# Kernel tuning notes

Measured on AMD Instinct MI355X. Metric: run time of the kernel, lower is better.

The kernel has to match this reference:

```python
import jax, jax.numpy as jnp
import numpy as np

B, S, HID = 4, 2048, 2048
H, KV, D = 16, 4, 128
G = H // KV  # kv groups
EPS = 1e-6
SCALE = D ** -0.5


def setup_inputs() -> dict:
    key = jax.random.key(0)
    ks = jax.random.split(key, 8)
    hidden_states = jax.random.normal(ks[0], (B, S, HID), jnp.float32)
    # real RoPE tables (rotate-half convention: freqs duplicated across halves)
    inv_freq = 1.0 / (10000.0 ** (np.arange(0, D, 2, dtype=np.float32) / D))
    t = np.arange(S, dtype=np.float32)
    freqs = np.outer(t, inv_freq)                      # [S, D/2]
    emb = np.concatenate([freqs, freqs], axis=-1)      # [S, D]
    cos = jnp.asarray(np.cos(emb), jnp.float32)
    sin = jnp.asarray(np.sin(emb), jnp.float32)
    std = HID ** -0.5
    Wq = jax.random.normal(ks[1], (HID, H * D), jnp.float32) * std
    Wk = jax.random.normal(ks[2], (HID, KV * D), jnp.float32) * std
    Wv = jax.random.normal(ks[3], (HID, KV * D), jnp.float32) * std
    Wo = jax.random.normal(ks[4], (H * D, HID), jnp.float32) * std
    q_norm_w = jnp.ones((D,), jnp.float32)
    k_norm_w = jnp.ones((D,), jnp.float32)
    return {"hidden_states": hidden_states, "cos": cos, "sin": sin,
            "Wq": Wq, "Wk": Wk, "Wv": Wv, "Wo": Wo,
            "q_norm_w": q_norm_w, "k_norm_w": k_norm_w}


def _rms_norm(x, w):
    xf = x.astype(jnp.float32)
    var = jnp.mean(xf * xf, axis=-1, keepdims=True)
    return w * (xf * jax.lax.rsqrt(var + EPS)).astype(x.dtype)


def _rotate_half(x):
    x1, x2 = x[..., : D // 2], x[..., D // 2:]
    return jnp.concatenate([-x2, x1], axis=-1)


def reference(hidden_states, cos, sin, Wq, Wk, Wv, Wo, q_norm_w, k_norm_w):
    x = hidden_states  # [B, S, HID]
    # projections + per-head RMSNorm
    q = _rms_norm((x @ Wq).reshape(B, S, H, D), q_norm_w).transpose(0, 2, 1, 3)   # [B,H,S,D]
    k = _rms_norm((x @ Wk).reshape(B, S, KV, D), k_norm_w).transpose(0, 2, 1, 3)  # [B,KV,S,D]
    v = (x @ Wv).reshape(B, S, KV, D).transpose(0, 2, 1, 3)                        # [B,KV,S,D]
    # RoPE (cos/sin broadcast [S,D] -> [B,heads,S,D])
    q = q * cos + _rotate_half(q) * sin
    k = k * cos + _rotate_half(k) * sin
    # GQA attention without materializing expanded K/V: group q heads per kv head
    qg = q.reshape(B, KV, G, S, D)
    scores = jnp.einsum('bkgsd,bktd->bkgst', qg, k) * SCALE       # [B,KV,G,S,S]
    probs = jax.nn.softmax(scores, axis=-1)
    out = jnp.einsum('bkgst,bktd->bkgsd', probs, v)               # [B,KV,G,S,D]
    out = out.reshape(B, H, S, D).transpose(0, 2, 1, 3).reshape(B, S, H * D)
    return out @ Wo
```

## Files before the change

kernel.cpp:

```cpp
#include <hip/hip_runtime.h>

#define DEVI __device__ __forceinline__

#define B_    4
#define S_    2048
#define HID_  2048
#define H_    16
#define KV_   4
#define D_    128
#define NQKV_ 3072
#define SCALE_ 0.08838834764831845f
#define L2E_   1.44269504088896340736f

typedef __bf16 bf16x8 __attribute__((ext_vector_type(8)));
typedef float  f32x4  __attribute__((ext_vector_type(4)));
typedef float  f32x16 __attribute__((ext_vector_type(16)));
typedef unsigned short ushort_t;

DEVI unsigned short f2bu(float f) {
  unsigned u = __float_as_uint(f);
  u += 0x7fffu + ((u >> 16) & 1u);
  return (unsigned short)(u >> 16);
}
DEVI float bu2f(unsigned short s) { return __uint_as_float(((unsigned)s) << 16); }
DEVI unsigned pk2(float a, float b) {
  return (unsigned)f2bu(a) | ((unsigned)f2bu(b) << 16);
}

DEVI void storev(ushort_t* p, float v) { *p = f2bu(v); }
DEVI void storev(float* p, float v)    { *p = v; }

DEVI void gl_lds16(const void* gptr, void* ldsptr) {
  __builtin_amdgcn_global_load_lds(
      (const __attribute__((address_space(1))) void*)gptr,
      (__attribute__((address_space(3))) void*)ldsptr, 16, 0, 0);
}

__global__ void k_cvt(const float* __restrict__ in, ushort_t* __restrict__ out, int n8) {
  int i = blockIdx.x * blockDim.x + threadIdx.x;
  if (i >= n8) return;
  const float4* p = (const float4*)in + (size_t)i * 2;
  float4 a = p[0], b = p[1];
  uint4 o;
  o.x = pk2(a.x, a.y);
  o.y = pk2(a.z, a.w);
  o.z = pk2(b.x, b.y);
  o.w = pk2(b.z, b.w);
  ((uint4*)out)[i] = o;
}

__global__ void k_transw(const float* __restrict__ in, ushort_t* __restrict__ out,
                         int K, int N) {
  __shared__ float tile[64][65];
  int k0 = blockIdx.x * 64, n0 = blockIdx.y * 64;
  int c = threadIdx.x & 63, r0 = threadIdx.x >> 6;
  #pragma unroll
  for (int i = 0; i < 16; ++i) {
    int r = r0 * 16 + i;
    tile[r][c] = in[(size_t)(k0 + r) * N + n0 + c];
  }
  __syncthreads();
  #pragma unroll
  for (int i = 0; i < 16; ++i) {
    int r = r0 * 16 + i;
    out[(size_t)(n0 + r) * K + k0 + c] = f2bu(tile[c][r]);
  }
}

__global__ void k_vtrans(const ushort_t* __restrict__ qkv, ushort_t* __restrict__ Vt) {
  __shared__ ushort_t tile[64][65];
  int s0 = blockIdx.x * 64, d0 = blockIdx.y * 64;
  int bkv = blockIdx.z, b = bkv >> 2, vh = bkv & 3;
  int c = threadIdx.x & 63, r0 = (threadIdx.x >> 6) * 16;
  const ushort_t* src = qkv + (size_t)(b * S_ + s0) * NQKV_ + 2560 + vh * 128 + d0;
  #pragma unroll
  for (int i = 0; i < 16; ++i) {
    int r = r0 + i;
    tile[r][c] = src[(size_t)r * NQKV_ + c];
  }
  __syncthreads();
  ushort_t* dst = Vt + ((size_t)(b * KV_ + vh) * D_ + d0) * S_ + s0;
  #pragma unroll
  for (int i = 0; i < 16; ++i) {
    int r = r0 + i;
    dst[(size_t)r * S_ + c] = tile[c][r];
  }
}

template <typename OutT>
__global__ __launch_bounds__(256)
void k_gemm(const ushort_t* __restrict__ A, const ushort_t* __restrict__ Bt,
            OutT* __restrict__ C, int M, int N, int K) {
  __shared__ __align__(16) ushort_t As[128 * 64];
  __shared__ __align__(16) ushort_t Bs[128 * 64];
  const int tid = threadIdx.x;
  const int wave = tid >> 6, lane = tid & 63;
  const int wr = wave >> 1, wc = wave & 1;
  const int h4 = lane >> 4, c16 = lane & 15;
  const int m0 = blockIdx.x * 128, n0 = blockIdx.y * 128;

  const int srow  = wave * 8 + (lane >> 3);
  const int scolb = (lane & 7) * 16;

  const ushort_t* Ap = A  + (size_t)m0 * K;
  const ushort_t* Bp = Bt + (size_t)n0 * K;

  f32x4 acc[4][4] = {};

  for (int kt = 0; kt < K; kt += 64) {
    __syncthreads();
    #pragma unroll
    for (int p = 0; p < 4; ++p) {
      int row = p * 32 + srow;
      gl_lds16((const char*)(Ap + (size_t)row * K + kt) + scolb,
               (char*)As + p * 4096 + wave * 1024);
      gl_lds16((const char*)(Bp + (size_t)row * K + kt) + scolb,
               (char*)Bs + p * 4096 + wave * 1024);
    }
    __syncthreads();
    #pragma unroll
    for (int kc = 0; kc < 2; ++kc) {
      bf16x8 af[4], bfr[4];
      #pragma unroll
      for (int m = 0; m < 4; ++m)
        af[m] = *(const bf16x8*)((const char*)As + (wr * 64 + m * 16 + c16) * 128 + kc * 64 + h4 * 16);
      #pragma unroll
      for (int n = 0; n < 4; ++n)
        bfr[n] = *(const bf16x8*)((const char*)Bs + (wc * 64 + n * 16 + c16) * 128 + kc * 64 + h4 * 16);
      #pragma unroll
      for (int m = 0; m < 4; ++m)
        #pragma unroll
        for (int n = 0; n < 4; ++n)
          acc[m][n] = __builtin_amdgcn_mfma_f32_16x16x32_bf16(af[m], bfr[n], acc[m][n], 0, 0, 0);
    }
  }
  #pragma unroll
  for (int m = 0; m < 4; ++m)
    #pragma unroll
    for (int n = 0; n < 4; ++n)
      #pragma unroll
      for (int r = 0; r < 4; ++r) {
        int grow = m0 + wr * 64 + m * 16 + h4 * 4 + r;
        int gcol = n0 + wc * 64 + n * 16 + c16;
        storev(&C[(size_t)grow * N + gcol], acc[m][n][r]);
      }
}

__global__ void k_normrope(const ushort_t* __restrict__ qkv,
                           const float* __restrict__ cosT, const float* __restrict__ sinT,
                           const float* __restrict__ qw, const float* __restrict__ kw,
                           ushort_t* __restrict__ Qr,
                           ushort_t* __restrict__ Kr) {
  int wid = blockIdx.x * 4 + (threadIdx.x >> 6);
  int lane = threadIdx.x & 63;
  int sub = wid % 20;
  int bs = wid / 20;
  int b = bs >> 11, s = bs & 2047;
  bool isQ = sub < 16;
  int head = isQ ? sub : sub - 16;
  const ushort_t* rp = qkv + (size_t)bs * NQKV_ + (isQ ? head * 128 : 2048 + head * 128);
  float e0 = bu2f(rp[lane]);
  float e1 = bu2f(rp[lane + 64]);
  float ss2 = e0 * e0 + e1 * e1;
  #pragma unroll
  for (int off = 32; off; off >>= 1) ss2 += __shfl_xor(ss2, off);
  float rinv = rsqrtf(ss2 * (1.0f / 128.0f) + 1e-6f);
  const float* w = isQ ? qw : kw;
  float y0 = e0 * rinv * w[lane];
  float y1 = e1 * rinv * w[lane + 64];
  float c0 = cosT[s * 128 + lane],      sn0 = sinT[s * 128 + lane];
  float c1 = cosT[s * 128 + lane + 64], sn1 = sinT[s * 128 + lane + 64];
  float o0 = y0 * c0 - y1 * sn0;
  float o1 = y1 * c1 + y0 * sn1;
  if (isQ) { o0 *= (SCALE_ * L2E_); o1 *= (SCALE_ * L2E_); }
  ushort_t* op = isQ ? (Qr + ((size_t)(b * H_ + head) * S_ + s) * D_)
                     : (Kr + ((size_t)(b * KV_ + head) * S_ + s) * D_);
  op[lane]      = f2bu(o0);
  op[lane + 64] = f2bu(o1);
}

__global__ __launch_bounds__(256, 2)
void k_attn(const ushort_t* __restrict__ Qr, const ushort_t* __restrict__ Kr,
            const ushort_t* __restrict__ Vt, ushort_t* __restrict__ AO) {
  __shared__ __align__(16) ushort_t Ks[2][64 * 128];
  __shared__ __align__(16) ushort_t Vs[2][128 * 64];
  const int bh = blockIdx.y;
  const int b = bh >> 4, h = bh & 15, kvh = h >> 2;
  const int q0 = blockIdx.x * 128;
  const int tid = threadIdx.x;
  const int wave = tid >> 6, lane = tid & 63;
  const int l31 = lane & 31, hi = lane >> 5;

  const ushort_t* qp = Qr + ((size_t)(b * H_ + h) * S_ + q0 + wave * 32 + l31) * D_;
  bf16x8 qf[8];
  #pragma unroll
  for (int kc = 0; kc < 8; ++kc)
    qf[kc] = *(const bf16x8*)(qp + kc * 16 + hi * 8);

  const ushort_t* Kg = Kr + (size_t)(b * KV_ + kvh) * S_ * D_;
  const ushort_t* Vg = Vt + (size_t)(b * KV_ + kvh) * D_ * S_;

  const int soff = wave * 1024 + lane * 16;

  float mrow = -1e30f, lsum = 0.0f;
  f32x16 Of[4] = {};

#define STAGE(bufi, s0)                                                        \
  {                                                                            \
    _Pragma("unroll")                                                          \
    for (int p = 0; p < 4; ++p) {                                              \
      int off = p * 4096 + soff;                                               \
      int krow = off >> 8, kcolb = off & 255;                                  \
      int ksc = kcolb ^ ((krow & 7) << 4);                                     \
      gl_lds16((const char*)(Kg + (size_t)((s0) + krow) * D_) + ksc,           \
               (char*)Ks[bufi] + p * 4096 + wave * 1024);                      \
      int vrow = off >> 7, vcolb = off & 127;                                  \
      int vsc = vcolb ^ ((vrow & 7) << 4);                                     \
      gl_lds16((const char*)(Vg + (size_t)vrow * S_ + (s0)) + vsc,             \
               (char*)Vs[bufi] + p * 4096 + wave * 1024);                      \
    }                                                                          \
  }

  STAGE(0, 0);
  asm volatile("s_waitcnt vmcnt(0)" ::: "memory");
  __builtin_amdgcn_s_barrier();

  for (int nt = 0; nt < S_ / 64; ++nt) {
    const int cur = nt & 1;
    if (nt + 1 < S_ / 64) STAGE(cur ^ 1, (nt + 1) * 64);

    f32x16 st[2] = {};
    __builtin_amdgcn_s_setprio(1);
    #pragma unroll
    for (int t = 0; t < 2; ++t) {
      const int row = t * 32 + l31;
      const int xr = (row & 7) << 4;
      #pragma unroll
      for (int kc = 0; kc < 8; ++kc) {
        bf16x8 kf = *(const bf16x8*)((const char*)Ks[cur] + row * 256 +
                                     ((kc * 32 + hi * 16) ^ xr));
        st[t] = __builtin_amdgcn_mfma_f32_32x32x16_bf16(kf, qf[kc], st[t], 0, 0, 0);
      }
    }
    __builtin_amdgcn_s_setprio(0);

    float tmax = st[0][0];
    #pragma unroll
    for (int r = 1; r < 16; ++r) tmax = fmaxf(tmax, st[0][r]);
    #pragma unroll
    for (int r = 0; r < 16; ++r) tmax = fmaxf(tmax, st[1][r]);
    tmax = fmaxf(tmax, __shfl_xor(tmax, 32));

    if (!__all(tmax - mrow <= 8.0f)) {
      const float mnew = fmaxf(mrow, tmax);
      const float corr = exp2f(mrow - mnew);
      #pragma unroll
      for (int dt = 0; dt < 4; ++dt)
        #pragma unroll
        for (int r = 0; r < 16; ++r) Of[dt][r] *= corr;
      lsum *= corr;
      mrow = mnew;
    }

    float psum = 0.0f;
    unsigned u[16];
    #pragma unroll
    for (int t = 0; t < 2; ++t)
      #pragma unroll
      for (int j = 0; j < 8; ++j) {
        float pa = exp2f(st[t][2 * j]     - mrow);
        float pb = exp2f(st[t][2 * j + 1] - mrow);
        psum += pa + pb;
        unsigned short xa = __builtin_bit_cast(unsigned short, (__bf16)pa);
        unsigned short xb = __builtin_bit_cast(unsigned short, (__bf16)pb);
        u[t * 8 + j] = (unsigned)xa | ((unsigned)xb << 16);
      }
    lsum += psum;

    #pragma unroll
    for (int kt = 0; kt < 4; ++kt) {
      const int base = (kt >> 1) * 8 + (kt & 1) * 4;
      unsigned w0 = u[base], w1 = u[base + 1], w2 = u[base + 2], w3 = u[base + 3];
      asm("v_permlane32_swap_b32 %0, %1" : "+v"(w0), "+v"(w2));
      asm("v_permlane32_swap_b32 %0, %1" : "+v"(w1), "+v"(w3));
      uint4 pw; pw.x = w0; pw.y = w1; pw.z = w2; pw.w = w3;
      bf16x8 pb = __builtin_bit_cast(bf16x8, pw);
      __builtin_amdgcn_s_setprio(1);
      #pragma unroll
      for (int dt = 0; dt < 4; ++dt) {
        const int row = dt * 32 + l31;
        bf16x8 vb = *(const bf16x8*)((const char*)Vs[cur] + row * 128 +
                                     ((kt * 32 + hi * 16) ^ ((row & 7) << 4)));
        Of[dt] = __builtin_amdgcn_mfma_f32_32x32x16_bf16(vb, pb, Of[dt], 0, 0, 0);
      }
      __builtin_amdgcn_s_setprio(0);
    }

    asm volatile("s_waitcnt vmcnt(0)" ::: "memory");
    __builtin_amdgcn_s_barrier();
  }
#undef STAGE

  lsum += __shfl_xor(lsum, 32);
  const float inv = 1.0f / lsum;

  const int s = q0 + wave * 32 + l31;
  ushort_t* aop = AO + ((size_t)(b * S_ + s) * H_ + h) * D_;
  #pragma unroll
  for (int dt = 0; dt < 4; ++dt)
    #pragma unroll
    for (int g = 0; g < 4; ++g) {
      const int d0 = dt * 32 + g * 8 + hi * 4;
      const int r0 = g * 4;
      uint2 o;
      o.x = pk2(Of[dt][r0]     * inv, Of[dt][r0 + 1] * inv);
      o.y = pk2(Of[dt][r0 + 2] * inv, Of[dt][r0 + 3] * inv);
      *(uint2*)(aop + d0) = o;
    }
}

extern "C" void kernel_launch(void* const* d_in, const int* in_sizes, int n_in,
                              void* d_out, int out_size, void* d_ws, size_t ws_size,
                              hipStream_t stream) {
  const float* x    = (const float*)d_in[0];
  const float* cosT = (const float*)d_in[1];
  const float* sinT = (const float*)d_in[2];
  const float* Wq   = (const float*)d_in[3];
  const float* Wk   = (const float*)d_in[4];
  const float* Wv   = (const float*)d_in[5];
  const float* Wo   = (const float*)d_in[6];
  const float* qw   = (const float*)d_in[7];
  const float* kw   = (const float*)d_in[8];
  float* out = (float*)d_out;

  char* ws = (char*)d_ws;
  ushort_t* Xb    = (ushort_t*)(ws + 0);
  ushort_t* QKVt  = (ushort_t*)(ws + 33554432);
  ushort_t* Wtqkv = (ushort_t*)(ws + 83886080);
  ushort_t* Wto   = (ushort_t*)(ws + 96468992);
  ushort_t* Kr    = (ushort_t*)(ws + 104857600);
  ushort_t* Vt    = (ushort_t*)(ws + 113246208);
  ushort_t* Qr = Xb;
  ushort_t* AO = QKVt;

  k_cvt<<<8192, 256, 0, stream>>>(x, Xb, 2097152);
  k_transw<<<dim3(32, 32), 256, 0, stream>>>(Wq, Wtqkv, 2048, 2048);
  k_transw<<<dim3(32, 8),  256, 0, stream>>>(Wk, Wtqkv + (size_t)2048 * 2048, 2048, 512);
  k_transw<<<dim3(32, 8),  256, 0, stream>>>(Wv, Wtqkv + (size_t)2560 * 2048, 2048, 512);
  k_transw<<<dim3(32, 32), 256, 0, stream>>>(Wo, Wto, 2048, 2048);
  k_gemm<ushort_t><<<dim3(64, 24), 256, 0, stream>>>(Xb, Wtqkv, QKVt, 8192, 3072, 2048);
  k_normrope<<<40960, 256, 0, stream>>>(QKVt, cosT, sinT, qw, kw, Qr, Kr);
  k_vtrans<<<dim3(32, 2, 16), 256, 0, stream>>>(QKVt, Vt);
  k_attn<<<dim3(16, 64), 256, 0, stream>>>(Qr, Kr, Vt, AO);
  k_gemm<float><<<dim3(64, 16), 256, 0, stream>>>(AO, Wto, out, 8192, 2048, 2048);
}
```

Baseline: 619.9 us.

## Swizzle GEMM and attention blocks across XCDs and single-buffer attention K/V tiles

Remaps block indices in the GEMM and attention kernels so that blocks sharing operands, such as the same batch/KV head or the same tile rows, land on the same XCD, to improve L2 reuse. The attention kernel also drops its K/V double buffer. It now loads each tile and synchronizes before computing, which halves LDS use, and the min-blocks launch bound is removed. This trades load/compute overlap for possibly higher occupancy and better cache locality. The swizzles assume grid sizes divisible by 8.

```diff
diff --git a/kernel.cpp b/kernel.cpp
--- a/kernel.cpp
+++ b/kernel.cpp
@@ -97,7 +97,11 @@
   const int wave = tid >> 6, lane = tid & 63;
   const int wr = wave >> 1, wc = wave & 1;
   const int h4 = lane >> 4, c16 = lane & 15;
-  const int m0 = blockIdx.x * 128, n0 = blockIdx.y * 128;
+
+  const int bid = blockIdx.y * gridDim.x + blockIdx.x;
+  const int cpx = (gridDim.x * gridDim.y) >> 3;
+  const int swz = (bid & 7) * cpx + (bid >> 3);
+  const int m0 = (swz % gridDim.x) * 128, n0 = (swz / gridDim.x) * 128;
 
   const int srow  = wave * 8 + (lane >> 3);
   const int scolb = (lane & 7) * 16;
@@ -179,14 +183,18 @@
   op[lane + 64] = f2bu(o1);
 }
 
-__global__ __launch_bounds__(256, 2)
+__global__ __launch_bounds__(256)
 void k_attn(const ushort_t* __restrict__ Qr, const ushort_t* __restrict__ Kr,
             const ushort_t* __restrict__ Vt, ushort_t* __restrict__ AO) {
-  __shared__ __align__(16) ushort_t Ks[2][64 * 128];
-  __shared__ __align__(16) ushort_t Vs[2][128 * 64];
-  const int bh = blockIdx.y;
+  __shared__ __align__(16) ushort_t Ks[64 * 128];
+  __shared__ __align__(16) ushort_t Vs[128 * 64];
+
+  const int bid0 = blockIdx.y * gridDim.x + blockIdx.x;
+  const int swzb = (bid0 & 7) * 128 + (bid0 >> 3);
+  const int bh = swzb >> 4;
   const int b = bh >> 4, h = bh & 15, kvh = h >> 2;
-  const int q0 = blockIdx.x * 128;
+  const int q0 = (swzb & 15) * 128;
+
   const int tid = threadIdx.x;
   const int wave = tid >> 6, lane = tid & 63;
   const int l31 = lane & 31, hi = lane >> 5;
@@ -205,29 +213,21 @@
   float mrow = -1e30f, lsum = 0.0f;
   f32x16 Of[4] = {};
 
-#define STAGE(bufi, s0)                                                        \
-  {                                                                            \
-    _Pragma("unroll")                                                          \
-    for (int p = 0; p < 4; ++p) {                                              \
-      int off = p * 4096 + soff;                                               \
-      int krow = off >> 8, kcolb = off & 255;                                  \
-      int ksc = kcolb ^ ((krow & 7) << 4);                                     \
-      gl_lds16((const char*)(Kg + (size_t)((s0) + krow) * D_) + ksc,           \
-               (char*)Ks[bufi] + p * 4096 + wave * 1024);                      \
-      int vrow = off >> 7, vcolb = off & 127;                                  \
-      int vsc = vcolb ^ ((vrow & 7) << 4);                                     \
-      gl_lds16((const char*)(Vg + (size_t)vrow * S_ + (s0)) + vsc,             \
-               (char*)Vs[bufi] + p * 4096 + wave * 1024);                      \
-    }                                                                          \
-  }
-
-  STAGE(0, 0);
-  asm volatile("s_waitcnt vmcnt(0)" ::: "memory");
-  __builtin_amdgcn_s_barrier();
-
   for (int nt = 0; nt < S_ / 64; ++nt) {
-    const int cur = nt & 1;
-    if (nt + 1 < S_ / 64) STAGE(cur ^ 1, (nt + 1) * 64);
+    const int s0 = nt * 64;
+    #pragma unroll
+    for (int p = 0; p < 4; ++p) {
+      int off = p * 4096 + soff;
+      int krow = off >> 8, kcolb = off & 255;
+      int ksc = kcolb ^ ((krow & 7) << 4);
+      gl_lds16((const char*)(Kg + (size_t)(s0 + krow) * D_) + ksc,
+               (char*)Ks + p * 4096 + wave * 1024);
+      int vrow = off >> 7, vcolb = off & 127;
+      int vsc = vcolb ^ ((vrow & 7) << 4);
+      gl_lds16((const char*)(Vg + (size_t)vrow * S_ + s0) + vsc,
+               (char*)Vs + p * 4096 + wave * 1024);
+    }
+    __syncthreads();
 
     f32x16 st[2] = {};
     __builtin_amdgcn_s_setprio(1);
@@ -237,7 +237,7 @@
       const int xr = (row & 7) << 4;
       #pragma unroll
       for (int kc = 0; kc < 8; ++kc) {
-        bf16x8 kf = *(const bf16x8*)((const char*)Ks[cur] + row * 256 +
+        bf16x8 kf = *(const bf16x8*)((const char*)Ks + row * 256 +
                                      ((kc * 32 + hi * 16) ^ xr));
         st[t] = __builtin_amdgcn_mfma_f32_32x32x16_bf16(kf, qf[kc], st[t], 0, 0, 0);
       }
@@ -289,17 +289,15 @@
       #pragma unroll
       for (int dt = 0; dt < 4; ++dt) {
         const int row = dt * 32 + l31;
-        bf16x8 vb = *(const bf16x8*)((const char*)Vs[cur] + row * 128 +
+        bf16x8 vb = *(const bf16x8*)((const char*)Vs + row * 128 +
                                      ((kt * 32 + hi * 16) ^ ((row & 7) << 4)));
         Of[dt] = __builtin_amdgcn_mfma_f32_32x32x16_bf16(vb, pb, Of[dt], 0, 0, 0);
       }
       __builtin_amdgcn_s_setprio(0);
     }
 
-    asm volatile("s_waitcnt vmcnt(0)" ::: "memory");
     __builtin_amdgcn_s_barrier();
   }
-#undef STAGE
 
   lsum += __shfl_xor(lsum, 32);
   const float inv = 1.0f / lsum;
```

Measured after the change: 613.1 us. About the same (-1.1%).
